# Kernel optimization log

Hardware: AMD Instinct MI355X
Metric: run time of the kernel (lower is better)

## Reference

```python
import jax, jax.numpy as jnp
import numpy as np

B, S, E, H = 2, 2048, 1024, 16
D = E // H  # head_dim = 64


def setup_inputs() -> dict:
    key = jax.random.key(0)
    ks = jax.random.split(key, 9)
    sc = 1.0 / np.sqrt(E)
    return {
        "x": jax.random.normal(ks[0], (B, S, E), dtype=jnp.float32),
        "Wq": jax.random.normal(ks[1], (E, E), dtype=jnp.float32) * sc,
        "bq": jnp.zeros((E,), dtype=jnp.float32),
        "Wk": jax.random.normal(ks[2], (E, E), dtype=jnp.float32) * sc,
        "bk": jnp.zeros((E,), dtype=jnp.float32),
        "Wv": jax.random.normal(ks[3], (E, E), dtype=jnp.float32) * sc,
        "bv": jnp.zeros((E,), dtype=jnp.float32),
        "Wo": jax.random.normal(ks[4], (E, E), dtype=jnp.float32) * sc,
        "bo": jnp.zeros((E,), dtype=jnp.float32),
    }


def reference(x, Wq, bq, Wk, bk, Wv, bv, Wo, bo):
    b, s, e = x.shape
    # projections: [B,S,E] -> [B,H,S,D]
    def heads(w, bias):
        return (x @ w + bias).reshape(b, s, H, D).transpose(0, 2, 1, 3)
    q, k, v = heads(Wq, bq), heads(Wk, bk), heads(Wv, bv)
    # scores [B,H,S,S]
    scores = jnp.einsum("bhqd,bhkd->bhqk", q, k) / jnp.sqrt(jnp.float32(D))
    causal = jnp.tril(jnp.ones((s, s), dtype=bool))
    scores = jnp.where(causal[None, None], scores, -jnp.inf)
    weights = jax.nn.softmax(scores, axis=-1)
    out = jnp.einsum("bhqk,bhkd->bhqd", weights, v)
    out = out.transpose(0, 2, 1, 3).reshape(b, s, e)
    return out @ Wo + bo
```

## Files before the change

kernel.cpp:

```cpp
#include <hip/hip_runtime.h>
#include <hip/hip_bf16.h>

#define B_SZ 2
#define S_LEN 2048
#define E_DIM 1024
#define NH 16
#define DH 64
#define M_ROWS (B_SZ * S_LEN)
#define QB 128
#define KVB 64

typedef __attribute__((ext_vector_type(8))) short short8;
typedef __attribute__((ext_vector_type(4))) float floatx4;
typedef __attribute__((ext_vector_type(4))) int intx4;

static __device__ __forceinline__ unsigned short f2bf(float f) {
    __hip_bfloat16 h = __float2bfloat16(f);
    return *reinterpret_cast<unsigned short*>(&h);
}
static __device__ __forceinline__ float bf2f(unsigned short u) {
    unsigned int v = ((unsigned int)u) << 16;
    return __builtin_bit_cast(float, v);
}
static __device__ __forceinline__ unsigned int pack2bf(float lo, float hi) {
    return (unsigned int)f2bf(lo) | ((unsigned int)f2bf(hi) << 16);
}

static __device__ __forceinline__ void gl2lds16(const void* g, void* l) {
    __builtin_amdgcn_global_load_lds((const __attribute__((address_space(1))) void*)g,
                                     (__attribute__((address_space(3))) void*)l, 16, 0, 0);
}

#define WAIT_VM0() asm volatile("s_waitcnt vmcnt(0)" ::: "memory")
#define WAIT_LGKM0() asm volatile("s_waitcnt lgkmcnt(0)" ::: "memory")

__global__ __launch_bounds__(256) void prep(const float* __restrict__ x,
                                            unsigned short* __restrict__ Xb,
                                            const float* __restrict__ W0,
                                            const float* __restrict__ W1,
                                            const float* __restrict__ W2,
                                            const float* __restrict__ W3,
                                            unsigned short* __restrict__ T0,
                                            unsigned short* __restrict__ T1,
                                            unsigned short* __restrict__ T2,
                                            unsigned short* __restrict__ T3) {
    __shared__ float tile[32][33];
    int bid = blockIdx.x;
    int t = threadIdx.x;
    if (bid < 4096) {
        int i = (bid * 256 + t) * 4;
        float4 v = *reinterpret_cast<const float4*>(x + i);
        ushort4 o;
        o.x = f2bf(v.x); o.y = f2bf(v.y); o.z = f2bf(v.z); o.w = f2bf(v.w);
        *reinterpret_cast<ushort4*>(Xb + i) = o;
        return;
    }
    int u = bid - 4096;
    int z = u >> 10, rest = u & 1023;
    int bx = (rest & 31) * 32, by = (rest >> 5) * 32;
    const float* W = (z == 0) ? W0 : (z == 1) ? W1 : (z == 2) ? W2 : W3;
    unsigned short* Wt = (z == 0) ? T0 : (z == 1) ? T1 : (z == 2) ? T2 : T3;
    int tx = t & 31, ty = t >> 5;
#pragma unroll
    for (int i = 0; i < 32; i += 8)
        tile[ty + i][tx] = W[(size_t)(by + ty + i) * E_DIM + bx + tx];
    __syncthreads();
#pragma unroll
    for (int i = 0; i < 32; i += 8)
        Wt[(size_t)(bx + ty + i) * E_DIM + by + tx] = f2bf(tile[tx][ty + i]);
}

#define QSCALE 0.18033688011112042f

__global__ __launch_bounds__(512, 2) void gemm_qkv8(const unsigned short* __restrict__ Wcat,
                                                    const unsigned short* __restrict__ Xb,
                                                    const float* __restrict__ bq,
                                                    const float* __restrict__ bk,
                                                    const float* __restrict__ bv,
                                                    unsigned short* __restrict__ Qg,
                                                    unsigned short* __restrict__ Kg,
                                                    unsigned short* __restrict__ Vtg) {
    __shared__ __align__(16) char lds[2][2][32768];

    int t = threadIdx.x;
    int b = blockIdx.x;
    int xcd = b & 7, ii = b >> 3;
    int it = (xcd & 3) * 3 + (ii >> 3);
    int jt = (xcd >> 2) * 8 + (ii & 7);
    int iBase = it << 8, jBase = jt << 8;

    int w = t >> 6, lane = t & 63;
    int lr = lane & 15, lh = lane >> 4;
    int wm = w >> 2, wn = w & 3;

    int srow = t >> 3;
    int scbx = ((t & 7) << 4) ^ ((srow & 7) << 4);

    const char* Ab = (const char*)Wcat;
    const char* Bb = (const char*)Xb;

    floatx4 acc[8][4];
#pragma unroll
    for (int i = 0; i < 8; i++)
#pragma unroll
        for (int j = 0; j < 4; j++) acc[i][j] = (floatx4){0.f, 0.f, 0.f, 0.f};

    auto stageA = [&](int buf, int kt) {
        int k0b = kt << 7;
#pragma unroll
        for (int c = 0; c < 4; c++)
            gl2lds16(Ab + (size_t)(iBase + c * 64 + srow) * 2048 + k0b + scbx,
                     &lds[buf][0][c * 8192 + t * 16]);
    };
    auto stageB = [&](int buf, int kt) {
        int k0b = kt << 7;
#pragma unroll
        for (int c = 0; c < 4; c++)
            gl2lds16(Bb + (size_t)(jBase + c * 64 + srow) * 2048 + k0b + scbx,
                     &lds[buf][1][c * 8192 + t * 16]);
    };

    short8 af[4][2], bf[4][2];
    auto rdA = [&](int buf, int qm) {
#pragma unroll
        for (int mi = 0; mi < 4; mi++)
#pragma unroll
            for (int ks = 0; ks < 2; ks++) {
                int row = wm * 128 + qm * 64 + mi * 16 + lr;
                af[mi][ks] = *reinterpret_cast<const short8*>(
                    &lds[buf][0][(row * 128 + ks * 64 + lh * 16) ^ ((row & 7) << 4)]);
            }
    };
    auto rdB = [&](int buf, int qn) {
#pragma unroll
        for (int ni = 0; ni < 2; ni++)
#pragma unroll
            for (int ks = 0; ks < 2; ks++) {
                int row = wn * 64 + qn * 32 + ni * 16 + lr;
                bf[qn * 2 + ni][ks] = *reinterpret_cast<const short8*>(
                    &lds[buf][1][(row * 128 + ks * 64 + lh * 16) ^ ((row & 7) << 4)]);
            }
    };
    auto mfma16 = [&](int qm, int qn) {
        __builtin_amdgcn_s_setprio(1);
#pragma unroll
        for (int mi = 0; mi < 4; mi++)
#pragma unroll
            for (int ni = 0; ni < 2; ni++)
#pragma unroll
                for (int ks = 0; ks < 2; ks++)
                    acc[qm * 4 + mi][qn * 2 + ni] = __builtin_amdgcn_mfma_f32_16x16x32_bf16(
                        af[mi][ks], bf[qn * 2 + ni][ks], acc[qm * 4 + mi][qn * 2 + ni], 0, 0, 0);
        __builtin_amdgcn_s_setprio(0);
    };

    const int NT = 16;
    stageA(0, 0);
    stageB(0, 0);
    WAIT_VM0();
    __builtin_amdgcn_s_barrier();

    for (int kt = 0; kt < NT; ++kt) {
        int cur = kt & 1, nxt = cur ^ 1;
        bool pf = (kt + 1 < NT);
        rdA(cur, 0);
        rdB(cur, 0);
        if (pf) stageA(nxt, kt + 1);
        __builtin_amdgcn_s_barrier();
        WAIT_LGKM0();
        __builtin_amdgcn_sched_barrier(0);
        mfma16(0, 0);
        __builtin_amdgcn_s_barrier();
        rdB(cur, 1);
        if (pf) stageB(nxt, kt + 1);
        __builtin_amdgcn_s_barrier();
        WAIT_LGKM0();
        __builtin_amdgcn_sched_barrier(0);
        mfma16(0, 1);
        __builtin_amdgcn_s_barrier();
        rdA(cur, 1);
        __builtin_amdgcn_s_barrier();
        WAIT_LGKM0();
        __builtin_amdgcn_sched_barrier(0);
        mfma16(1, 0);
        __builtin_amdgcn_s_barrier();
        if (pf) WAIT_VM0();
        __builtin_amdgcn_s_barrier();
        mfma16(1, 1);
        __builtin_amdgcn_s_barrier();
    }

    int wsel = iBase >> 10;
    const float* bias = (wsel == 0) ? bq : (wsel == 1) ? bk : bv;
    __syncthreads();

    if (wsel < 2) {
        unsigned short* O = wsel ? Kg : Qg;
        float scale = wsel ? 1.0f : QSCALE;
#pragma unroll
        for (int mi8 = 0; mi8 < 8; mi8++) {
            int i = iBase + wm * 128 + mi8 * 16 + lh * 4;
            int im = i & 1023;
            int h = im >> 6, d0 = im & 63;
            float4 bs = *reinterpret_cast<const float4*>(&bias[im]);
#pragma unroll
            for (int nf = 0; nf < 4; nf++) {
                int j = jBase + wn * 64 + nf * 16 + lr;
                int b_ = j >> 11, s = j & (S_LEN - 1);
                ushort4 pk;
                pk.x = f2bf((acc[mi8][nf][0] + bs.x) * scale);
                pk.y = f2bf((acc[mi8][nf][1] + bs.y) * scale);
                pk.z = f2bf((acc[mi8][nf][2] + bs.z) * scale);
                pk.w = f2bf((acc[mi8][nf][3] + bs.w) * scale);
                *reinterpret_cast<ushort4*>(
                    &O[((size_t)(b_ * NH + h) * S_LEN + s) * DH + d0]) = pk;
            }
        }
    } else {
        char* lw = &lds[0][0][0] + w * 16384;
#pragma unroll
        for (int mi8 = 0; mi8 < 8; mi8++) {
            int i = iBase + wm * 128 + mi8 * 16 + lh * 4;
            float4 bs = *reinterpret_cast<const float4*>(&bias[i & 1023]);
#pragma unroll
            for (int nf = 0; nf < 4; nf++) {
                int jl = nf * 16 + lr;
#pragma unroll
                for (int r = 0; r < 4; r++) {
                    int il = mi8 * 16 + lh * 4 + r;
                    float bb = (r == 0) ? bs.x : (r == 1) ? bs.y : (r == 2) ? bs.z : bs.w;
                    *reinterpret_cast<unsigned short*>(
                        lw + ((il * 128 + jl * 2) ^ ((il & 7) << 4))) =
                        f2bf(acc[mi8][nf][r] + bb);
                }
            }
        }
        __syncthreads();
#pragma unroll
        for (int rep = 0; rep < 16; rep++) {
            int idx = rep * 64 + lane;
            int il = idx >> 3, jb = idx & 7;
            short8 vv = *reinterpret_cast<const short8*>(
                lw + ((il * 128 + jb * 16) ^ ((il & 7) << 4)));
            int i = iBase + wm * 128 + il;
            int im = i & 1023;
            int h = im >> 6, d = im & 63;
            int j = jBase + wn * 64 + jb * 8;
            int b_ = j >> 11, s = j & (S_LEN - 1);
            *reinterpret_cast<short8*>(
                &Vtg[((size_t)(b_ * NH + h) * DH + d) * S_LEN + s]) = vv;
        }
    }
}

template <int NI>
static __device__ __forceinline__ void gemm_tile_mainloop(
    const unsigned short* __restrict__ A, const unsigned short* __restrict__ Bt,
    int mBase, int nBase, char* ldsA, char* ldsB, floatx4 (&acc)[4][NI]) {
    const int K = E_DIM;
    int t = threadIdx.x;
    int w = t >> 6, lane = t & 63;
    int lr = lane & 15, lh = lane >> 4;
    int wm = w >> 1, wn = w & 1;
    const char* Ab = (const char*)A;
    const char* Bb = (const char*)Bt;
    int srow = t >> 3;
    int scb = ((t & 7) << 4) ^ ((srow & 7) << 4);

#pragma unroll
    for (int mi = 0; mi < 4; mi++)
#pragma unroll
        for (int ni = 0; ni < NI; ni++) acc[mi][ni] = (floatx4){0.f, 0.f, 0.f, 0.f};

    for (int kt = 0; kt < K / 64; ++kt) {
        int k0 = kt * 64;
#pragma unroll
        for (int i = 0; i < 4; i++)
            gl2lds16(Ab + (size_t)(mBase + i * 32 + srow) * (K * 2) + k0 * 2 + scb,
                     ldsA + i * 4096 + t * 16);
#pragma unroll
        for (int i = 0; i < NI; i++)
            gl2lds16(Bb + (size_t)(nBase + i * 32 + srow) * (K * 2) + k0 * 2 + scb,
                     ldsB + i * 4096 + t * 16);
        __syncthreads();
#pragma unroll
        for (int ks = 0; ks < 2; ks++) {
            short8 af[4], bfr[NI];
#pragma unroll
            for (int mi = 0; mi < 4; mi++) {
                int row = wm * 64 + mi * 16 + lr;
                af[mi] = *reinterpret_cast<const short8*>(
                    ldsA + ((row * 128 + ks * 64 + lh * 16) ^ ((row & 7) << 4)));
            }
#pragma unroll
            for (int ni = 0; ni < NI; ni++) {
                int row = wn * (NI * 16) + ni * 16 + lr;
                bfr[ni] = *reinterpret_cast<const short8*>(
                    ldsB + ((row * 128 + ks * 64 + lh * 16) ^ ((row & 7) << 4)));
            }
#pragma unroll
            for (int mi = 0; mi < 4; mi++)
#pragma unroll
                for (int ni = 0; ni < NI; ni++)
                    acc[mi][ni] = __builtin_amdgcn_mfma_f32_16x16x32_bf16(af[mi], bfr[ni],
                                                                          acc[mi][ni], 0, 0, 0);
        }
        __syncthreads();
    }
}

__global__ __launch_bounds__(256) void gemm_o(const unsigned short* __restrict__ Og,
                                              const unsigned short* __restrict__ Wot,
                                              const float* __restrict__ bo,
                                              float* __restrict__ out) {
    __shared__ __align__(16) char ldsA[16384];
    __shared__ __align__(16) char ldsB[8192];
    int bid = blockIdx.y * 16 + blockIdx.x;
    int xcd = bid & 7, ii = bid >> 3;
    int xx = ii & 15;
    int yy = (xcd << 2) | (ii >> 4);
    int nBase = xx << 6;
    int mBase = yy << 7;

    floatx4 acc[4][2];
    gemm_tile_mainloop<2>(Og, Wot, mBase, nBase, ldsA, ldsB, acc);

    int w = threadIdx.x >> 6, lane = threadIdx.x & 63;
    int lr = lane & 15, lh = lane >> 4;
    int wm = w >> 1, wn = w & 1;
#pragma unroll
    for (int mi = 0; mi < 4; mi++)
#pragma unroll
        for (int ni = 0; ni < 2; ni++)
#pragma unroll
            for (int r = 0; r < 4; r++) {
                int m = mBase + wm * 64 + mi * 16 + lh * 4 + r;
                int n = nBase + wn * 32 + ni * 16 + lr;
                out[(size_t)m * E_DIM + n] = acc[mi][ni][r] + bo[n];
            }
}

__global__ __launch_bounds__(256, 4) void attn_fwd(const unsigned short* __restrict__ Qg,
                                                   const unsigned short* __restrict__ Kg,
                                                   const unsigned short* __restrict__ Vtg,
                                                   unsigned short* __restrict__ Og,
                                                   unsigned short* __restrict__ Opart,
                                                   float* __restrict__ lpart) {
    __shared__ __align__(16) char kt_lds[2][KVB * 128];
    __shared__ __align__(16) char vt_lds[2][KVB * 128];

    int bid = blockIdx.x;
    int xcd = bid & 7, ii = bid >> 3;
    int bh = (xcd << 2) + ii / 30;
    int jj = 29 - (ii % 30);
    int qb, ch, c;
    if (jj < 6)        { qb = jj; ch = 0; c = 1; }
    else if (jj < 18)  { int u = jj - 6;  qb = 6 + (u >> 1); ch = u & 1; c = 2; }
    else               { int u = jj - 18; qb = 12 + u / 3;   ch = u % 3; c = 3; }
    int T = 2 * qb + 2;
    int kt_lo = ch * T / c;
    int kt_hi = (ch + 1) * T / c - 1;
    bool split = (c > 1);

    int w = threadIdx.x >> 6, lane = threadIdx.x & 63;
    int lr = lane & 15, lh = lane >> 4;
    int q0 = qb * QB + w * 32;

    const char* Kb = (const char*)(Kg + (size_t)bh * S_LEN * DH);
    const char* Vb = (const char*)(Vtg + (size_t)bh * DH * S_LEN);
    const unsigned short* Qb = Qg + (size_t)bh * S_LEN * DH;

    int wi0 = w * 2;
    int srow0 = wi0 * 8 + (lane >> 3);
    int scol = (lane & 7) << 4;

    auto stage = [&](int buf, int kt) {
        int kv0 = kt * KVB;
#pragma unroll
        for (int i = 0; i < 2; ++i) {
            int row = srow0 + i * 8;
            int colb = scol ^ ((row & 7) << 4);
            gl2lds16(Kb + (size_t)(kv0 + row) * 128 + colb,
                     kt_lds[buf] + (wi0 + i) * 1024);
            gl2lds16(Vb + (size_t)row * (S_LEN * 2) + (size_t)kv0 * 2 + colb,
                     vt_lds[buf] + (wi0 + i) * 1024);
        }
    };

    short8 aq[2][2];
#pragma unroll
    for (int m = 0; m < 2; m++)
#pragma unroll
        for (int ks = 0; ks < 2; ks++)
            aq[m][ks] = *reinterpret_cast<const short8*>(
                Qb + (size_t)(q0 + m * 16 + lr) * DH + ks * 32 + lh * 8);

    floatx4 oacc[2][4];
    float lsum[2];
#pragma unroll
    for (int m = 0; m < 2; m++) {
#pragma unroll
        for (int dt = 0; dt < 4; dt++) oacc[m][dt] = (floatx4){0.f, 0.f, 0.f, 0.f};
        lsum[m] = 0.f;
    }

    stage(0, kt_lo);
    __syncthreads();
    int buf = 0;

    for (int kt = kt_lo; kt <= kt_hi; ++kt) {
        if (kt < kt_hi) stage(buf ^ 1, kt + 1);
        int kv0 = kt * KVB;
        bool skip = (kv0 > q0 + 31);
        if (!skip) {
            const char* Kt = kt_lds[buf];
            const char* Vt = vt_lds[buf];
            floatx4 sacc[2][4];
#pragma unroll
            for (int m = 0; m < 2; m++)
#pragma unroll
                for (int nt = 0; nt < 4; nt++) sacc[m][nt] = (floatx4){0.f, 0.f, 0.f, 0.f};
#pragma unroll
            for (int ks = 0; ks < 2; ks++)
#pragma unroll
                for (int nt = 0; nt < 4; nt++) {
                    int row = nt * 16 + lr;
                    int addr = (row * 128 + ks * 64 + lh * 16) ^ ((row & 7) << 4);
                    short8 bk = *reinterpret_cast<const short8*>(Kt + addr);
#pragma unroll
                    for (int m = 0; m < 2; m++)
                        sacc[m][nt] = __builtin_amdgcn_mfma_f32_16x16x32_bf16(
                            bk, aq[m][ks], sacc[m][nt], 0, 0, 0);
                }
            if (kv0 + KVB - 1 > q0) {
#pragma unroll
                for (int m = 0; m < 2; m++)
#pragma unroll
                    for (int nt = 0; nt < 4; nt++)
#pragma unroll
                        for (int r = 0; r < 4; r++) {
                            int kcol = kv0 + nt * 16 + lh * 4 + r;
                            int qrow = q0 + m * 16 + lr;
                            if (kcol > qrow) sacc[m][nt][r] = -1e30f;
                        }
            }
            unsigned int pk[2][4][2];
#pragma unroll
            for (int m = 0; m < 2; m++) {
                float ls = 0.f;
#pragma unroll
                for (int nt = 0; nt < 4; nt++) {
#pragma unroll
                    for (int r = 0; r < 4; r++) {
                        float p = __builtin_amdgcn_exp2f(sacc[m][nt][r]);
                        sacc[m][nt][r] = p;
                        ls += p;
                    }
                    pk[m][nt][0] = pack2bf(sacc[m][nt][0], sacc[m][nt][1]);
                    pk[m][nt][1] = pack2bf(sacc[m][nt][2], sacc[m][nt][3]);
                }
                lsum[m] += ls;
            }
            short8 pa[2][2];
            int hsel = lh >> 1;
#pragma unroll
            for (int m = 0; m < 2; m++)
#pragma unroll
                for (int ks = 0; ks < 2; ks++) {
                    intx4 u;
#pragma unroll
                    for (int t4 = 0; t4 < 4; t4++) {
                        int src = lr + 32 * (lh & 1) + 16 * (t4 >> 1);
                        int r0 = __shfl((int)pk[m][2 * ks][t4 & 1], src);
                        int r1 = __shfl((int)pk[m][2 * ks + 1][t4 & 1], src);
                        u[t4] = hsel ? r1 : r0;
                    }
                    pa[m][ks] = __builtin_bit_cast(short8, u);
                }
#pragma unroll
            for (int ks = 0; ks < 2; ks++)
#pragma unroll
                for (int dt = 0; dt < 4; dt++) {
                    int row = dt * 16 + lr;
                    int addr = (row * 128 + ks * 64 + lh * 16) ^ ((row & 7) << 4);
                    short8 bv = *reinterpret_cast<const short8*>(Vt + addr);
#pragma unroll
                    for (int m = 0; m < 2; m++)
                        oacc[m][dt] = __builtin_amdgcn_mfma_f32_16x16x32_bf16(
                            pa[m][ks], bv, oacc[m][dt], 0, 0, 0);
                }
        }
        __syncthreads();
        buf ^= 1;
    }

#pragma unroll
    for (int m = 0; m < 2; m++) {
        lsum[m] += __shfl_xor(lsum[m], 16);
        lsum[m] += __shfl_xor(lsum[m], 32);
    }

    if (split) {
        int base = (qb < 12) ? (qb - 6) * 2 : 12 + (qb - 12) * 3;
        int pi = bh * 24 + base + ch;
        unsigned short* Op = Opart + (size_t)pi * (QB * DH);
        float* lp = lpart + (size_t)pi * QB;
#pragma unroll
        for (int m = 0; m < 2; m++) {
            if (lh == 0) lp[w * 32 + m * 16 + lr] = lsum[m];
#pragma unroll
            for (int r = 0; r < 4; r++) {
                int row = w * 32 + m * 16 + lh * 4 + r;
#pragma unroll
                for (int dt = 0; dt < 4; dt++)
                    Op[row * DH + dt * 16 + lr] = f2bf(oacc[m][dt][r]);
            }
        }
    } else {
        int b_ = bh >> 4, h_ = bh & 15;
#pragma unroll
        for (int m = 0; m < 2; m++) {
#pragma unroll
            for (int r = 0; r < 4; r++) {
                float lv = __shfl(lsum[m], lh * 4 + r);
                float inv = 1.f / lv;
                int srow = q0 + m * 16 + lh * 4 + r;
#pragma unroll
                for (int dt = 0; dt < 4; dt++)
                    Og[((size_t)b_ * S_LEN + srow) * E_DIM + h_ * 64 + dt * 16 + lr] =
                        f2bf(oacc[m][dt][r] * inv);
            }
        }
    }
}

__global__ __launch_bounds__(256) void attn_reduce(const unsigned short* __restrict__ Opart,
                                                   const float* __restrict__ lpart,
                                                   unsigned short* __restrict__ Og) {
    int bh = blockIdx.x;
    int qb = 6 + blockIdx.y;
    int c = (qb < 12) ? 2 : 3;
    int base = (qb < 12) ? (qb - 6) * 2 : 12 + (qb - 12) * 3;
    int pi0 = bh * 24 + base;
    const unsigned short* P0 = Opart + (size_t)pi0 * (QB * DH);
    const float* l0 = lpart + (size_t)pi0 * QB;
    int t = threadIdx.x;
    int cg = t & 7, r0 = t >> 3;
    int b_ = bh >> 4, h_ = bh & 15;
    int qrow0 = qb * QB;
#pragma unroll
    for (int rr = 0; rr < 4; rr++) {
        int row = r0 + rr * 32;
        float ls = l0[row] + l0[QB + row];
        if (c == 3) ls += l0[2 * QB + row];
        float inv = 1.f / ls;
        short8 v0 = *reinterpret_cast<const short8*>(P0 + row * DH + cg * 8);
        short8 v1 = *reinterpret_cast<const short8*>(P0 + QB * DH + row * DH + cg * 8);
        float s[8];
#pragma unroll
        for (int j = 0; j < 8; j++)
            s[j] = bf2f((unsigned short)v0[j]) + bf2f((unsigned short)v1[j]);
        if (c == 3) {
            short8 v2 = *reinterpret_cast<const short8*>(P0 + 2 * QB * DH + row * DH + cg * 8);
#pragma unroll
            for (int j = 0; j < 8; j++) s[j] += bf2f((unsigned short)v2[j]);
        }
        short8 o;
#pragma unroll
        for (int j = 0; j < 8; j++) o[j] = (short)f2bf(s[j] * inv);
        *reinterpret_cast<short8*>(Og + ((size_t)b_ * S_LEN + qrow0 + row) * E_DIM +
                                   h_ * 64 + cg * 8) = o;
    }
}

extern "C" void kernel_launch(void* const* d_in, const int* in_sizes, int n_in,
                              void* d_out, int out_size, void* d_ws, size_t ws_size,
                              hipStream_t stream) {
    const float* x  = (const float*)d_in[0];
    const float* Wq = (const float*)d_in[1];
    const float* bq = (const float*)d_in[2];
    const float* Wk = (const float*)d_in[3];
    const float* bk = (const float*)d_in[4];
    const float* Wv = (const float*)d_in[5];
    const float* bv = (const float*)d_in[6];
    const float* Wo = (const float*)d_in[7];
    const float* bo = (const float*)d_in[8];
    float* out = (float*)d_out;

    const size_t NX = (size_t)M_ROWS * E_DIM;
    const size_t NW = (size_t)E_DIM * E_DIM;
    unsigned short* ws  = (unsigned short*)d_ws;
    unsigned short* Xb  = ws;
    unsigned short* Wqt = Xb + NX;
    unsigned short* Wkt = Wqt + NW;
    unsigned short* Wvt = Wkt + NW;
    unsigned short* Wot = Wvt + NW;
    unsigned short* Qg  = Wot + NW;
    unsigned short* Kg  = Qg + NX;
    unsigned short* Vtg = Kg + NX;
    unsigned short* Og  = Vtg + NX;
    unsigned short* Opart = Xb;
    float* lpart = (float*)(Opart + (size_t)32 * 24 * QB * DH);

    prep<<<dim3(8192), 256, 0, stream>>>(x, Xb, Wq, Wk, Wv, Wo, Wqt, Wkt, Wvt, Wot);

    gemm_qkv8<<<dim3(192), 512, 0, stream>>>(Wqt, Xb, bq, bk, bv, Qg, Kg, Vtg);

    attn_fwd<<<dim3(960), 256, 0, stream>>>(Qg, Kg, Vtg, Og, Opart, lpart);
    attn_reduce<<<dim3(B_SZ * NH, 10), 256, 0, stream>>>(Opart, lpart, Og);

    gemm_o<<<dim3(E_DIM / 64, M_ROWS / 128), 256, 0, stream>>>(Og, Wot, bo, out);
}
```

Before: 113.6 us.

## Enlarge attention query tile to 256 rows with new split-KV partition

Doubles the per-block query tile from 128 to 256 rows (each wave handles 64 rows), so every staged K/V tile feeds twice as many MFMAs. A new split-KV schedule spreads the work over 736 blocks and writes partials into two workspace regions. The reduce kernel is generalized to combine 2 to 5 partials per row. Register pressure rises and occupancy drops to 2 waves per SIMD, and the larger tiles waste more work on the causal diagonal.

New measurement: 125.7 us. 1.11x slower.

```diff
diff --git a/kernel.cpp b/kernel.cpp
--- a/kernel.cpp
+++ b/kernel.cpp
@@ -7,7 +7,6 @@
 #define NH 16
 #define DH 64
 #define M_ROWS (B_SZ * S_LEN)
-#define QB 128
 #define KVB 64
 
 typedef __attribute__((ext_vector_type(8))) short short8;
@@ -340,31 +339,37 @@
             }
 }
 
-__global__ __launch_bounds__(256, 4) void attn_fwd(const unsigned short* __restrict__ Qg,
+__global__ __launch_bounds__(256, 2) void attn_fwd(const unsigned short* __restrict__ Qg,
                                                    const unsigned short* __restrict__ Kg,
                                                    const unsigned short* __restrict__ Vtg,
                                                    unsigned short* __restrict__ Og,
-                                                   unsigned short* __restrict__ Opart,
+                                                   unsigned short* __restrict__ OpA,
+                                                   unsigned short* __restrict__ OpB,
                                                    float* __restrict__ lpart) {
     __shared__ __align__(16) char kt_lds[2][KVB * 128];
     __shared__ __align__(16) char vt_lds[2][KVB * 128];
 
     int bid = blockIdx.x;
     int xcd = bid & 7, ii = bid >> 3;
-    int bh = (xcd << 2) + ii / 30;
-    int jj = 29 - (ii % 30);
-    int qb, ch, c;
-    if (jj < 6)        { qb = jj; ch = 0; c = 1; }
-    else if (jj < 18)  { int u = jj - 6;  qb = 6 + (u >> 1); ch = u & 1; c = 2; }
-    else               { int u = jj - 18; qb = 12 + u / 3;   ch = u % 3; c = 3; }
-    int T = 2 * qb + 2;
+    int bh = (xcd << 2) + ii / 23;
+    int jj = ii % 23;
+    int qb, ch, c, base;
+    if (jj < 5)        { qb = 7; ch = jj;      c = 5; base = 16; }
+    else if (jj < 9)   { qb = 6; ch = jj - 5;  c = 4; base = 12; }
+    else if (jj < 13)  { qb = 5; ch = jj - 9;  c = 4; base = 8;  }
+    else if (jj < 16)  { qb = 4; ch = jj - 13; c = 3; base = 5;  }
+    else if (jj < 19)  { qb = 3; ch = jj - 16; c = 3; base = 2;  }
+    else if (jj < 21)  { qb = 2; ch = jj - 19; c = 2; base = 0;  }
+    else if (jj == 21) { qb = 1; ch = 0;       c = 1; base = 0;  }
+    else               { qb = 0; ch = 0;       c = 1; base = 0;  }
+    int T = 4 * qb + 4;
     int kt_lo = ch * T / c;
     int kt_hi = (ch + 1) * T / c - 1;
     bool split = (c > 1);
 
     int w = threadIdx.x >> 6, lane = threadIdx.x & 63;
     int lr = lane & 15, lh = lane >> 4;
-    int q0 = qb * QB + w * 32;
+    int q0 = qb * 256 + w * 64;
 
     const char* Kb = (const char*)(Kg + (size_t)bh * S_LEN * DH);
     const char* Vb = (const char*)(Vtg + (size_t)bh * DH * S_LEN);
@@ -387,18 +392,18 @@
         }
     };
 
-    short8 aq[2][2];
-#pragma unroll
-    for (int m = 0; m < 2; m++)
+    short8 aq[4][2];
+#pragma unroll
+    for (int m = 0; m < 4; m++)
 #pragma unroll
         for (int ks = 0; ks < 2; ks++)
             aq[m][ks] = *reinterpret_cast<const short8*>(
                 Qb + (size_t)(q0 + m * 16 + lr) * DH + ks * 32 + lh * 8);
 
-    floatx4 oacc[2][4];
-    float lsum[2];
-#pragma unroll
-    for (int m = 0; m < 2; m++) {
+    floatx4 oacc[4][4];
+    float lsum[4];
+#pragma unroll
+    for (int m = 0; m < 4; m++) {
 #pragma unroll
         for (int dt = 0; dt < 4; dt++) oacc[m][dt] = (floatx4){0.f, 0.f, 0.f, 0.f};
         lsum[m] = 0.f;
@@ -411,13 +416,13 @@
     for (int kt = kt_lo; kt <= kt_hi; ++kt) {
         if (kt < kt_hi) stage(buf ^ 1, kt + 1);
         int kv0 = kt * KVB;
-        bool skip = (kv0 > q0 + 31);
+        bool skip = (kv0 > q0 + 63);
         if (!skip) {
             const char* Kt = kt_lds[buf];
             const char* Vt = vt_lds[buf];
-            floatx4 sacc[2][4];
-#pragma unroll
-            for (int m = 0; m < 2; m++)
+            floatx4 sacc[4][4];
+#pragma unroll
+            for (int m = 0; m < 4; m++)
 #pragma unroll
                 for (int nt = 0; nt < 4; nt++) sacc[m][nt] = (floatx4){0.f, 0.f, 0.f, 0.f};
 #pragma unroll
@@ -428,13 +433,13 @@
                     int addr = (row * 128 + ks * 64 + lh * 16) ^ ((row & 7) << 4);
                     short8 bk = *reinterpret_cast<const short8*>(Kt + addr);
 #pragma unroll
-                    for (int m = 0; m < 2; m++)
+                    for (int m = 0; m < 4; m++)
                         sacc[m][nt] = __builtin_amdgcn_mfma_f32_16x16x32_bf16(
                             bk, aq[m][ks], sacc[m][nt], 0, 0, 0);
                 }
             if (kv0 + KVB - 1 > q0) {
 #pragma unroll
-                for (int m = 0; m < 2; m++)
+                for (int m = 0; m < 4; m++)
 #pragma unroll
                     for (int nt = 0; nt < 4; nt++)
 #pragma unroll
@@ -444,9 +449,10 @@
                             if (kcol > qrow) sacc[m][nt][r] = -1e30f;
                         }
             }
-            unsigned int pk[2][4][2];
-#pragma unroll
-            for (int m = 0; m < 2; m++) {
+            int hsel = lh >> 1;
+#pragma unroll
+            for (int m = 0; m < 4; m++) {
+                unsigned int pk[4][2];
                 float ls = 0.f;
 #pragma unroll
                 for (int nt = 0; nt < 4; nt++) {
@@ -456,61 +462,56 @@
                         sacc[m][nt][r] = p;
                         ls += p;
                     }
-                    pk[m][nt][0] = pack2bf(sacc[m][nt][0], sacc[m][nt][1]);
-                    pk[m][nt][1] = pack2bf(sacc[m][nt][2], sacc[m][nt][3]);
+                    pk[nt][0] = pack2bf(sacc[m][nt][0], sacc[m][nt][1]);
+                    pk[nt][1] = pack2bf(sacc[m][nt][2], sacc[m][nt][3]);
                 }
                 lsum[m] += ls;
-            }
-            short8 pa[2][2];
-            int hsel = lh >> 1;
-#pragma unroll
-            for (int m = 0; m < 2; m++)
+                short8 pa[2];
 #pragma unroll
                 for (int ks = 0; ks < 2; ks++) {
                     intx4 u;
 #pragma unroll
                     for (int t4 = 0; t4 < 4; t4++) {
                         int src = lr + 32 * (lh & 1) + 16 * (t4 >> 1);
-                        int r0 = __shfl((int)pk[m][2 * ks][t4 & 1], src);
-                        int r1 = __shfl((int)pk[m][2 * ks + 1][t4 & 1], src);
+                        int r0 = __shfl((int)pk[2 * ks][t4 & 1], src);
+                        int r1 = __shfl((int)pk[2 * ks + 1][t4 & 1], src);
                         u[t4] = hsel ? r1 : r0;
                     }
-                    pa[m][ks] = __builtin_bit_cast(short8, u);
+                    pa[ks] = __builtin_bit_cast(short8, u);
                 }
 #pragma unroll
-            for (int ks = 0; ks < 2; ks++)
-#pragma unroll
-                for (int dt = 0; dt < 4; dt++) {
-                    int row = dt * 16 + lr;
-                    int addr = (row * 128 + ks * 64 + lh * 16) ^ ((row & 7) << 4);
-                    short8 bv = *reinterpret_cast<const short8*>(Vt + addr);
-#pragma unroll
-                    for (int m = 0; m < 2; m++)
+                for (int ks = 0; ks < 2; ks++)
+#pragma unroll
+                    for (int dt = 0; dt < 4; dt++) {
+                        int row = dt * 16 + lr;
+                        int addr = (row * 128 + ks * 64 + lh * 16) ^ ((row & 7) << 4);
+                        short8 bv = *reinterpret_cast<const short8*>(Vt + addr);
                         oacc[m][dt] = __builtin_amdgcn_mfma_f32_16x16x32_bf16(
-                            pa[m][ks], bv, oacc[m][dt], 0, 0, 0);
-                }
+                            pa[ks], bv, oacc[m][dt], 0, 0, 0);
+                    }
+            }
         }
         __syncthreads();
         buf ^= 1;
     }
 
 #pragma unroll
-    for (int m = 0; m < 2; m++) {
+    for (int m = 0; m < 4; m++) {
         lsum[m] += __shfl_xor(lsum[m], 16);
         lsum[m] += __shfl_xor(lsum[m], 32);
     }
 
     if (split) {
-        int base = (qb < 12) ? (qb - 6) * 2 : 12 + (qb - 12) * 3;
-        int pi = bh * 24 + base + ch;
-        unsigned short* Op = Opart + (size_t)pi * (QB * DH);
-        float* lp = lpart + (size_t)pi * QB;
-#pragma unroll
-        for (int m = 0; m < 2; m++) {
-            if (lh == 0) lp[w * 32 + m * 16 + lr] = lsum[m];
+        int pi = bh * 21 + base + ch;
+        unsigned short* Op = (pi < 448) ? OpA + (size_t)pi * 16384
+                                        : OpB + (size_t)(pi - 448) * 16384;
+        float* lp = lpart + (size_t)pi * 256;
+#pragma unroll
+        for (int m = 0; m < 4; m++) {
+            if (lh == 0) lp[w * 64 + m * 16 + lr] = lsum[m];
 #pragma unroll
             for (int r = 0; r < 4; r++) {
-                int row = w * 32 + m * 16 + lh * 4 + r;
+                int row = w * 64 + m * 16 + lh * 4 + r;
 #pragma unroll
                 for (int dt = 0; dt < 4; dt++)
                     Op[row * DH + dt * 16 + lr] = f2bf(oacc[m][dt][r]);
@@ -519,7 +520,7 @@
     } else {
         int b_ = bh >> 4, h_ = bh & 15;
 #pragma unroll
-        for (int m = 0; m < 2; m++) {
+        for (int m = 0; m < 4; m++) {
 #pragma unroll
             for (int r = 0; r < 4; r++) {
                 float lv = __shfl(lsum[m], lh * 4 + r);
@@ -534,37 +535,35 @@
     }
 }
 
-__global__ __launch_bounds__(256) void attn_reduce(const unsigned short* __restrict__ Opart,
+__global__ __launch_bounds__(256) void attn_reduce(const unsigned short* __restrict__ OpA,
+                                                   const unsigned short* __restrict__ OpB,
                                                    const float* __restrict__ lpart,
                                                    unsigned short* __restrict__ Og) {
     int bh = blockIdx.x;
-    int qb = 6 + blockIdx.y;
-    int c = (qb < 12) ? 2 : 3;
-    int base = (qb < 12) ? (qb - 6) * 2 : 12 + (qb - 12) * 3;
-    int pi0 = bh * 24 + base;
-    const unsigned short* P0 = Opart + (size_t)pi0 * (QB * DH);
-    const float* l0 = lpart + (size_t)pi0 * QB;
+    int qy = blockIdx.y;
+    const int ctab[6] = {2, 3, 3, 4, 4, 5};
+    const int btab[6] = {0, 2, 5, 8, 12, 16};
+    int c = ctab[qy], base = btab[qy];
+    int pi0 = bh * 21 + base;
     int t = threadIdx.x;
     int cg = t & 7, r0 = t >> 3;
     int b_ = bh >> 4, h_ = bh & 15;
-    int qrow0 = qb * QB;
-#pragma unroll
-    for (int rr = 0; rr < 4; rr++) {
+    int qrow0 = (2 + qy) * 256;
+#pragma unroll
+    for (int rr = 0; rr < 8; rr++) {
         int row = r0 + rr * 32;
-        float ls = l0[row] + l0[QB + row];
-        if (c == 3) ls += l0[2 * QB + row];
+        float ls = 0.f;
+        float s[8] = {0.f, 0.f, 0.f, 0.f, 0.f, 0.f, 0.f, 0.f};
+        for (int k = 0; k < c; k++) {
+            int pi = pi0 + k;
+            const unsigned short* P = (pi < 448) ? OpA + (size_t)pi * 16384
+                                                 : OpB + (size_t)(pi - 448) * 16384;
+            ls += lpart[(size_t)pi * 256 + row];
+            short8 v = *reinterpret_cast<const short8*>(P + row * DH + cg * 8);
+#pragma unroll
+            for (int j = 0; j < 8; j++) s[j] += bf2f((unsigned short)v[j]);
+        }
         float inv = 1.f / ls;
-        short8 v0 = *reinterpret_cast<const short8*>(P0 + row * DH + cg * 8);
-        short8 v1 = *reinterpret_cast<const short8*>(P0 + QB * DH + row * DH + cg * 8);
-        float s[8];
-#pragma unroll
-        for (int j = 0; j < 8; j++)
-            s[j] = bf2f((unsigned short)v0[j]) + bf2f((unsigned short)v1[j]);
-        if (c == 3) {
-            short8 v2 = *reinterpret_cast<const short8*>(P0 + 2 * QB * DH + row * DH + cg * 8);
-#pragma unroll
-            for (int j = 0; j < 8; j++) s[j] += bf2f((unsigned short)v2[j]);
-        }
         short8 o;
 #pragma unroll
         for (int j = 0; j < 8; j++) o[j] = (short)f2bf(s[j] * inv);
@@ -599,15 +598,16 @@
     unsigned short* Kg  = Qg + NX;
     unsigned short* Vtg = Kg + NX;
     unsigned short* Og  = Vtg + NX;
-    unsigned short* Opart = Xb;
-    float* lpart = (float*)(Opart + (size_t)32 * 24 * QB * DH);
+    unsigned short* OpA = Xb;
+    unsigned short* OpB = Og + NX;
+    float* lpart = (float*)(OpB + (size_t)224 * 16384);
 
     prep<<<dim3(8192), 256, 0, stream>>>(x, Xb, Wq, Wk, Wv, Wo, Wqt, Wkt, Wvt, Wot);
 
     gemm_qkv8<<<dim3(192), 512, 0, stream>>>(Wqt, Xb, bq, bk, bv, Qg, Kg, Vtg);
 
-    attn_fwd<<<dim3(960), 256, 0, stream>>>(Qg, Kg, Vtg, Og, Opart, lpart);
-    attn_reduce<<<dim3(B_SZ * NH, 10), 256, 0, stream>>>(Opart, lpart, Og);
+    attn_fwd<<<dim3(736), 256, 0, stream>>>(Qg, Kg, Vtg, Og, OpA, OpB, lpart);
+    attn_reduce<<<dim3(B_SZ * NH, 6), 256, 0, stream>>>(OpA, OpB, lpart, Og);
 
     gemm_o<<<dim3(E_DIM / 64, M_ROWS / 128), 256, 0, stream>>>(Og, Wot, bo, out);
 }
```

## Rewrite output projection GEMM as double-buffered 512-thread pipelined kernel

Applied to the files above, without the earlier changes.

Replaces the simple single-buffered output-projection GEMM with an 8-wave kernel using 128x128 tiles and K-step 64 (128 bytes). The new kernel double-buffers LDS and interleaves global-to-LDS prefetch with MFMA work, raising wave priority around MFMAs. It computes the transposed product (Wo^T times O) so that each lane writes a float4 of consecutive output columns. The aim is to hide memory latency and cut the per-step barrier stalls of the old loop. In exchange it uses more LDS per block, issues more barriers per step, and launches only 256 blocks.

New measurement: 113.9 us, median of 2. No clear change (+0.3%).

```diff
diff --git a/kernel.cpp b/kernel.cpp
--- a/kernel.cpp
+++ b/kernel.cpp
@@ -253,91 +253,129 @@
     }
 }
 
-template <int NI>
-static __device__ __forceinline__ void gemm_tile_mainloop(
-    const unsigned short* __restrict__ A, const unsigned short* __restrict__ Bt,
-    int mBase, int nBase, char* ldsA, char* ldsB, floatx4 (&acc)[4][NI]) {
-    const int K = E_DIM;
+__global__ __launch_bounds__(512, 2) void gemm_o8(const unsigned short* __restrict__ Wot,
+                                                  const unsigned short* __restrict__ Og,
+                                                  const float* __restrict__ bo,
+                                                  float* __restrict__ out) {
+    __shared__ __align__(16) char lds[2][2][16384];
+
     int t = threadIdx.x;
+    int b = blockIdx.x;
+    int xcd = b & 7, ii = b >> 3;
+    int it = ii & 7;
+    int jt = (xcd << 2) | (ii >> 3);
+    int iBase = it << 7, jBase = jt << 7;
+
     int w = t >> 6, lane = t & 63;
     int lr = lane & 15, lh = lane >> 4;
-    int wm = w >> 1, wn = w & 1;
-    const char* Ab = (const char*)A;
-    const char* Bb = (const char*)Bt;
+    int wm = w >> 2, wn = w & 3;
+
     int srow = t >> 3;
-    int scb = ((t & 7) << 4) ^ ((srow & 7) << 4);
-
-#pragma unroll
-    for (int mi = 0; mi < 4; mi++)
-#pragma unroll
-        for (int ni = 0; ni < NI; ni++) acc[mi][ni] = (floatx4){0.f, 0.f, 0.f, 0.f};
-
-    for (int kt = 0; kt < K / 64; ++kt) {
-        int k0 = kt * 64;
-#pragma unroll
-        for (int i = 0; i < 4; i++)
-            gl2lds16(Ab + (size_t)(mBase + i * 32 + srow) * (K * 2) + k0 * 2 + scb,
-                     ldsA + i * 4096 + t * 16);
-#pragma unroll
-        for (int i = 0; i < NI; i++)
-            gl2lds16(Bb + (size_t)(nBase + i * 32 + srow) * (K * 2) + k0 * 2 + scb,
-                     ldsB + i * 4096 + t * 16);
-        __syncthreads();
-#pragma unroll
-        for (int ks = 0; ks < 2; ks++) {
-            short8 af[4], bfr[NI];
-#pragma unroll
-            for (int mi = 0; mi < 4; mi++) {
+    int scbx = ((t & 7) << 4) ^ ((srow & 7) << 4);
+
+    const char* Ab = (const char*)Wot;
+    const char* Bb = (const char*)Og;
+
+    floatx4 acc[4][2];
+#pragma unroll
+    for (int i = 0; i < 4; i++)
+#pragma unroll
+        for (int j = 0; j < 2; j++) acc[i][j] = (floatx4){0.f, 0.f, 0.f, 0.f};
+
+    auto stageA = [&](int buf, int kt) {
+        int k0b = kt << 7;
+#pragma unroll
+        for (int c = 0; c < 2; c++)
+            gl2lds16(Ab + (size_t)(iBase + c * 64 + srow) * 2048 + k0b + scbx,
+                     &lds[buf][0][c * 8192 + t * 16]);
+    };
+    auto stageB = [&](int buf, int kt) {
+        int k0b = kt << 7;
+#pragma unroll
+        for (int c = 0; c < 2; c++)
+            gl2lds16(Bb + (size_t)(jBase + c * 64 + srow) * 2048 + k0b + scbx,
+                     &lds[buf][1][c * 8192 + t * 16]);
+    };
+
+    short8 af[4][2], bf[2][2];
+    auto rdA = [&](int buf, int qm) {
+#pragma unroll
+        for (int m2 = 0; m2 < 2; m2++)
+#pragma unroll
+            for (int ks = 0; ks < 2; ks++) {
+                int mi = qm * 2 + m2;
                 int row = wm * 64 + mi * 16 + lr;
-                af[mi] = *reinterpret_cast<const short8*>(
-                    ldsA + ((row * 128 + ks * 64 + lh * 16) ^ ((row & 7) << 4)));
-            }
-#pragma unroll
-            for (int ni = 0; ni < NI; ni++) {
-                int row = wn * (NI * 16) + ni * 16 + lr;
-                bfr[ni] = *reinterpret_cast<const short8*>(
-                    ldsB + ((row * 128 + ks * 64 + lh * 16) ^ ((row & 7) << 4)));
-            }
-#pragma unroll
-            for (int mi = 0; mi < 4; mi++)
-#pragma unroll
-                for (int ni = 0; ni < NI; ni++)
-                    acc[mi][ni] = __builtin_amdgcn_mfma_f32_16x16x32_bf16(af[mi], bfr[ni],
-                                                                          acc[mi][ni], 0, 0, 0);
-        }
-        __syncthreads();
-    }
-}
-
-__global__ __launch_bounds__(256) void gemm_o(const unsigned short* __restrict__ Og,
-                                              const unsigned short* __restrict__ Wot,
-                                              const float* __restrict__ bo,
-                                              float* __restrict__ out) {
-    __shared__ __align__(16) char ldsA[16384];
-    __shared__ __align__(16) char ldsB[8192];
-    int bid = blockIdx.y * 16 + blockIdx.x;
-    int xcd = bid & 7, ii = bid >> 3;
-    int xx = ii & 15;
-    int yy = (xcd << 2) | (ii >> 4);
-    int nBase = xx << 6;
-    int mBase = yy << 7;
-
-    floatx4 acc[4][2];
-    gemm_tile_mainloop<2>(Og, Wot, mBase, nBase, ldsA, ldsB, acc);
-
-    int w = threadIdx.x >> 6, lane = threadIdx.x & 63;
-    int lr = lane & 15, lh = lane >> 4;
-    int wm = w >> 1, wn = w & 1;
-#pragma unroll
-    for (int mi = 0; mi < 4; mi++)
-#pragma unroll
-        for (int ni = 0; ni < 2; ni++)
-#pragma unroll
-            for (int r = 0; r < 4; r++) {
-                int m = mBase + wm * 64 + mi * 16 + lh * 4 + r;
-                int n = nBase + wn * 32 + ni * 16 + lr;
-                out[(size_t)m * E_DIM + n] = acc[mi][ni][r] + bo[n];
-            }
+                af[mi][ks] = *reinterpret_cast<const short8*>(
+                    &lds[buf][0][(row * 128 + ks * 64 + lh * 16) ^ ((row & 7) << 4)]);
+            }
+    };
+    auto rdB = [&](int buf) {
+#pragma unroll
+        for (int nf = 0; nf < 2; nf++)
+#pragma unroll
+            for (int ks = 0; ks < 2; ks++) {
+                int row = wn * 32 + nf * 16 + lr;
+                bf[nf][ks] = *reinterpret_cast<const short8*>(
+                    &lds[buf][1][(row * 128 + ks * 64 + lh * 16) ^ ((row & 7) << 4)]);
+            }
+    };
+    auto mfma8 = [&](int qm) {
+        __builtin_amdgcn_s_setprio(1);
+#pragma unroll
+        for (int m2 = 0; m2 < 2; m2++)
+#pragma unroll
+            for (int nf = 0; nf < 2; nf++)
+#pragma unroll
+                for (int ks = 0; ks < 2; ks++) {
+                    int mi = qm * 2 + m2;
+                    acc[mi][nf] = __builtin_amdgcn_mfma_f32_16x16x32_bf16(
+                        af[mi][ks], bf[nf][ks], acc[mi][nf], 0, 0, 0);
+                }
+        __builtin_amdgcn_s_setprio(0);
+    };
+
+    const int NT = 16;
+    stageA(0, 0);
+    stageB(0, 0);
+    WAIT_VM0();
+    __builtin_amdgcn_s_barrier();
+
+    for (int kt = 0; kt < NT; ++kt) {
+        int cur = kt & 1, nxt = cur ^ 1;
+        bool pf = (kt + 1 < NT);
+        rdA(cur, 0);
+        rdB(cur);
+        if (pf) stageA(nxt, kt + 1);
+        __builtin_amdgcn_s_barrier();
+        WAIT_LGKM0();
+        __builtin_amdgcn_sched_barrier(0);
+        mfma8(0);
+        __builtin_amdgcn_s_barrier();
+        rdA(cur, 1);
+        if (pf) stageB(nxt, kt + 1);
+        __builtin_amdgcn_s_barrier();
+        WAIT_LGKM0();
+        __builtin_amdgcn_sched_barrier(0);
+        mfma8(1);
+        if (pf) WAIT_VM0();
+        __builtin_amdgcn_s_barrier();
+    }
+
+#pragma unroll
+    for (int mi = 0; mi < 4; mi++) {
+        int i = iBase + wm * 64 + mi * 16 + lh * 4;
+        float4 bs = *reinterpret_cast<const float4*>(&bo[i]);
+#pragma unroll
+        for (int nf = 0; nf < 2; nf++) {
+            int j = jBase + wn * 32 + nf * 16 + lr;
+            float4 o;
+            o.x = acc[mi][nf][0] + bs.x;
+            o.y = acc[mi][nf][1] + bs.y;
+            o.z = acc[mi][nf][2] + bs.z;
+            o.w = acc[mi][nf][3] + bs.w;
+            *reinterpret_cast<float4*>(&out[(size_t)j * E_DIM + i]) = o;
+        }
+    }
 }
 
 __global__ __launch_bounds__(256, 4) void attn_fwd(const unsigned short* __restrict__ Qg,
@@ -609,5 +647,5 @@
     attn_fwd<<<dim3(960), 256, 0, stream>>>(Qg, Kg, Vtg, Og, Opart, lpart);
     attn_reduce<<<dim3(B_SZ * NH, 10), 256, 0, stream>>>(Opart, lpart, Og);
 
-    gemm_o<<<dim3(E_DIM / 64, M_ROWS / 128), 256, 0, stream>>>(Og, Wot, bo, out);
-}
+    gemm_o8<<<dim3(256), 512, 0, stream>>>(Wot, Og, bo, out);
+}
```
